# Performance work log

Hardware: AMD Instinct MI355X
Metric: run time of the kernel (lower is better)

Reference implementation:

```python
import jax, jax.numpy as jnp
import numpy as np

EPS = 1e-5  # torch BatchNorm2d default


def _conv5x5(x, w, b):
    # x: [N,1,H,W], w: [1,1,5,5], b: [1]; stride 1, padding 2 (SAME)
    out = jax.lax.conv_general_dilated(
        x, w, window_strides=(1, 1), padding=((2, 2), (2, 2)),
        dimension_numbers=("NCHW", "OIHW", "NCHW"))
    return out + b[None, :, None, None]


def _batchnorm(x, gamma, beta):
    # training-mode BatchNorm2d: per-channel batch stats over (N,H,W), biased var
    mean = jnp.mean(x, axis=(0, 2, 3), keepdims=True)
    var = jnp.mean(jnp.square(x - mean), axis=(0, 2, 3), keepdims=True)
    xhat = (x - mean) * jax.lax.rsqrt(var + EPS)
    return xhat * gamma[None, :, None, None] + beta[None, :, None, None]


def _shrinkage(x, lumdb):
    return x + 0.5 * (jnp.sqrt(jnp.square(x - lumdb) + 1.0)
                      - jnp.sqrt(jnp.square(x + lumdb) + 1.0))


def setup_inputs() -> dict:
    key = jax.random.key(0)
    k1, k2, k3 = jax.random.split(key, 3)
    y = jax.random.normal(k1, (64, 1, 512, 512), dtype=jnp.float32)
    # kaiming-uniform-ish init for a 1x1x5x5 conv
    fan_in = 25.0
    bound = 1.0 / np.sqrt(fan_in)
    conv_w = jax.random.uniform(k2, (1, 1, 5, 5), jnp.float32, -bound, bound)
    conv_b = jax.random.uniform(k3, (1,), jnp.float32, -bound, bound)
    gamma = jnp.ones((1,), jnp.float32)
    beta = jnp.zeros((1,), jnp.float32)
    lambd = jnp.array([2.0, 1.0, 0.0], jnp.float32)
    return {"y": y, "conv_w": conv_w, "conv_b": conv_b,
            "gamma": gamma, "beta": beta, "lambd": lambd}


def reference(y, conv_w, conv_b, gamma, beta, lambd):
    x_k = y
    # unrolled LISTA iteration 1
    x = _batchnorm(_conv5x5(x_k, conv_w, conv_b), gamma, beta)
    x = _shrinkage(x, lambd[0])
    o12 = _batchnorm(_conv5x5(x, conv_w, conv_b), gamma, beta)
    x = _batchnorm(_conv5x5(x_k, conv_w, conv_b), gamma, beta)
    # iteration 2
    x = _shrinkage(o12 + x, lambd[1])
    o22 = _batchnorm(_conv5x5(x, conv_w, conv_b), gamma, beta)
    x = _batchnorm(_conv5x5(x_k, conv_w, conv_b), gamma, beta)
    # iteration 3
    x = _shrinkage(o22 + x, lambd[2])
    return x
```

## Files before the change

kernel.cpp:

```cpp
#include <hip/hip_runtime.h>
#include <math.h>

#define HH 512
#define WW 512
#define NTOT (64u*512u*512u)
#define NBLK 1024
#define TS 128
#define TROWS 132
#define TCH 18
#define TPIT 152
#define NTASK (TROWS*TCH)
#define NITER 10

typedef __attribute__((ext_vector_type(8))) short short8;
typedef __attribute__((ext_vector_type(4))) float f32x4;

__device__ __forceinline__ float fsqrtf(float x) { return __builtin_amdgcn_sqrtf(x); }

__device__ __forceinline__ float shrinkf(float x, float l) {
    float a = x - l, b = x + l;
    return x + 0.5f * (fsqrtf(__builtin_fmaf(a, a, 1.f)) - fsqrtf(__builtin_fmaf(b, b, 1.f)));
}

__device__ __forceinline__ float bf2f(unsigned int u) {
    union { unsigned int i; float f; } cv;
    cv.i = u << 16;
    return cv.f;
}
__device__ __forceinline__ float lo2f(unsigned int p) {
    union { unsigned int i; float f; } cv; cv.i = p << 16; return cv.f;
}
__device__ __forceinline__ float hi2f(unsigned int p) {
    union { unsigned int i; float f; } cv; cv.i = p & 0xffff0000u; return cv.f;
}

__device__ __forceinline__ unsigned int cvtpk(float lo, float hi) {
    unsigned int r;
    asm("v_cvt_pk_bf16_f32 %0, %1, %2" : "=v"(r) : "v"(lo), "v"(hi));
    return r;
}

__device__ __forceinline__ void bf8(uint4 u, float* f) {
    f[0] = bf2f(u.x & 0xffffu); f[1] = bf2f(u.x >> 16);
    f[2] = bf2f(u.y & 0xffffu); f[3] = bf2f(u.y >> 16);
    f[4] = bf2f(u.z & 0xffffu); f[5] = bf2f(u.z >> 16);
    f[6] = bf2f(u.w & 0xffffu); f[7] = bf2f(u.w >> 16);
}

__device__ __forceinline__ void stats_reduce(
    const float* __restrict__ part, double* rs, double* rq, int tid,
    float gam, float bet, float& scl_out, float& shf_out)
{
    double sd = 0.0, qd = 0.0;
#pragma unroll
    for (int k = 0; k < 4; k++) {
        const int i = tid + k * 256;
        sd += (double)part[2 * i];
        qd += (double)part[2 * i + 1];
    }
    rs[tid] = sd; rq[tid] = qd;
    __syncthreads();
    for (int off = 128; off > 0; off >>= 1) {
        if (tid < off) { rs[tid] += rs[tid + off]; rq[tid] += rq[tid + off]; }
        __syncthreads();
    }
    const double mean = rs[0] / (double)NTOT;
    const double var  = rq[0] / (double)NTOT - mean * mean;
    const double scl  = (double)gam / sqrt(var + 1e-5);
    scl_out = (float)scl;
    shf_out = (float)((double)bet - mean * scl);
    __syncthreads();
}

template <int MODE, bool OBF>
__global__ __launch_bounds__(256, 4) void conv_k(
    const float* __restrict__ yin,
    const unsigned short* __restrict__ t1,
    const unsigned short* __restrict__ t2,
    unsigned short* __restrict__ outbf,
    float* __restrict__ outf32,
    const float* __restrict__ wgt,
    const float* __restrict__ bias,
    const float* __restrict__ prevPart,
    const float* __restrict__ statsIn,
    float* __restrict__ statsOut,
    const float* __restrict__ gamma,
    const float* __restrict__ beta,
    const float* __restrict__ lambd,
    float* __restrict__ partials)
{
    __shared__ unsigned short tile[TROWS * TPIT];

    const int tid = threadIdx.x;
    const int by = blockIdx.y * TS;
    const int bx = blockIdx.x * TS;
    const size_t ibase = (size_t)blockIdx.z * (HH * WW);

    float wloc[25];
#pragma unroll
    for (int i = 0; i < 25; i++) wloc[i] = wgt[i];

    const int lane = tid & 63;
    const int lm = lane & 15;
    const int kb = lane >> 4;
    const int basei = kb * 8 - lm - 6;
    short8 bfr[5];
#pragma unroll
    for (int ky = 0; ky < 5; ky++) {
        unsigned pkw[4];
#pragma unroll
        for (int jj = 0; jj < 4; jj++) {
            float v0 = 0.f, v1 = 0.f;
            const int i0 = basei + 2 * jj, i1 = i0 + 1;
#pragma unroll
            for (int t = 0; t < 5; t++) {
                if (i0 == t) v0 = wloc[ky * 5 + t];
                if (i1 == t) v1 = wloc[ky * 5 + t];
            }
            pkw[jj] = cvtpk(v0, v1);
        }
        union { unsigned u[4]; short8 s; } cv;
        cv.u[0] = pkw[0]; cv.u[1] = pkw[1]; cv.u[2] = pkw[2]; cv.u[3] = pkw[3];
        bfr[ky] = cv.s;
    }

    auto loadT = [&](int task, uint4& A, uint4& B) {
        A = make_uint4(0u,0u,0u,0u); B = make_uint4(0u,0u,0u,0u);
        const int row = task / TCH;
        const int ch  = task - row * TCH;
        const int gy  = by + row - 2;
        const int gx0 = bx + ch * 8 - 8;
        if (task < NTASK && gy >= 0 && gy < HH && gx0 >= 0 && gx0 <= WW - 8) {
            const size_t g = ibase + (size_t)gy * WW + gx0;
            if constexpr (MODE == 0) {
                A = *(const uint4*)(yin + g);
                B = *(const uint4*)(yin + g + 4);
            } else if constexpr (MODE == 1) {
                A = *(const uint4*)(t1 + g);
            } else {
                A = *(const uint4*)(t1 + g);
                B = *(const uint4*)(t2 + g);
            }
        }
    };

    uint4 sA0, sB0, sA1, sB1, sA2, sB2;
    loadT(tid,        sA0, sB0);
    loadT(tid + 256,  sA1, sB1);
    loadT(tid + 512,  sA2, sB2);

    float s1 = 0.f, h1 = 0.f, s2v = 0.f, h2 = 0.f, lam = 0.f;
    if constexpr (MODE == 1) {
        stats_reduce(prevPart, (double*)tile, ((double*)tile) + 256, tid,
                     gamma[0], beta[0], s1, h1);
        lam = lambd[0];
        if (tid == 0 && blockIdx.x == 0 && blockIdx.y == 0 && blockIdx.z == 0) {
            statsOut[0] = s1; statsOut[1] = h1;
        }
    }
    if constexpr (MODE == 2) {
        stats_reduce(prevPart, (double*)tile, ((double*)tile) + 256, tid,
                     gamma[0], beta[0], s2v, h2);
        s1 = statsIn[0]; h1 = statsIn[1];
        lam = lambd[1];
    }

    auto procT = [&](int task, uint4 A, uint4 B) {
        const int row = task / TCH;
        const int ch  = task - row * TCH;
        uint4 pk = make_uint4(0u,0u,0u,0u);
        if constexpr (MODE == 0) {
            const float4 a = *(const float4*)&A;
            const float4 b = *(const float4*)&B;
            pk.x = cvtpk(a.x, a.y); pk.y = cvtpk(a.z, a.w);
            pk.z = cvtpk(b.x, b.y); pk.w = cvtpk(b.z, b.w);
        } else if constexpr (MODE == 1) {
            float f1[8]; bf8(A, f1);
            float v[8];
#pragma unroll
            for (int k = 0; k < 8; k++)
                v[k] = shrinkf(__builtin_fmaf(f1[k], s1, h1), lam);
            pk.x = cvtpk(v[0], v[1]); pk.y = cvtpk(v[2], v[3]);
            pk.z = cvtpk(v[4], v[5]); pk.w = cvtpk(v[6], v[7]);
        } else {
            float f1[8], f2[8]; bf8(A, f1); bf8(B, f2);
            float v[8];
#pragma unroll
            for (int k = 0; k < 8; k++) {
                float x = __builtin_fmaf(f2[k], s2v, h2)
                        + __builtin_fmaf(f1[k], s1, h1);
                v[k] = shrinkf(x, lam);
            }
            pk.x = cvtpk(v[0], v[1]); pk.y = cvtpk(v[2], v[3]);
            pk.z = cvtpk(v[4], v[5]); pk.w = cvtpk(v[6], v[7]);
        }
        const int gy  = by + row - 2;
        const int gx0 = bx + ch * 8 - 8;
        if (!(gy >= 0 && gy < HH && gx0 >= 0 && gx0 <= WW - 8))
            pk = make_uint4(0u,0u,0u,0u);
        *(uint4*)&tile[row * TPIT + ch * 8] = pk;
    };

#pragma unroll
    for (int t = 0; t < NITER; t++) {
        const int task = tid + t * 256;
        if (task < NTASK) procT(task, sA0, sB0);
        sA0 = sA1; sB0 = sB1;
        sA1 = sA2; sB1 = sB2;
        if (t + 3 < NITER) {
            loadT(tid + (t + 3) * 256, sA2, sB2);
        } else {
            sA2 = make_uint4(0u,0u,0u,0u); sB2 = make_uint4(0u,0u,0u,0u);
        }
    }

    const float b0 = bias[0];
    __syncthreads();

    const int wv = tid >> 6;
    const int r0w = wv * 32;

    f32x4 acc[2][8];
#pragma unroll
    for (int st = 0; st < 2; st++)
#pragma unroll
        for (int ct = 0; ct < 8; ct++)
            acc[st][ct] = (f32x4){0.f, 0.f, 0.f, 0.f};

#pragma unroll
    for (int ky = 0; ky < 5; ky++) {
        const short8 b = bfr[ky];
#pragma unroll
        for (int st = 0; st < 2; st++) {
            const unsigned short* ab = &tile[(r0w + st * 16 + lm + ky) * TPIT + kb * 8];
#pragma unroll
            for (int ct = 0; ct < 8; ct++) {
                short8 a = *(const short8*)(ab + ct * 16);
                acc[st][ct] = __builtin_amdgcn_mfma_f32_16x16x32_bf16(a, b, acc[st][ct], 0, 0, 0);
            }
        }
    }

    float s = 0.f, q = 0.f;
#pragma unroll
    for (int st = 0; st < 2; st++) {
#pragma unroll
        for (int ct = 0; ct < 8; ct++) {
            const f32x4 a = acc[st][ct];
            const int grow0 = by + r0w + st * 16 + kb * 4;
            const size_t base = ibase + (size_t)grow0 * WW + bx + ct * 16 + lm;
            if constexpr (OBF) {
                unsigned p01 = cvtpk(a[0] + b0, a[1] + b0);
                unsigned p23 = cvtpk(a[2] + b0, a[3] + b0);
                outbf[base]          = (unsigned short)(p01 & 0xffffu);
                outbf[base + WW]     = (unsigned short)(p01 >> 16);
                outbf[base + 2 * WW] = (unsigned short)(p23 & 0xffffu);
                outbf[base + 3 * WW] = (unsigned short)(p23 >> 16);
                float fr0 = lo2f(p01), fr1 = hi2f(p01), fr2 = lo2f(p23), fr3 = hi2f(p23);
                s += fr0 + fr1 + fr2 + fr3;
                q = __builtin_fmaf(fr0, fr0, __builtin_fmaf(fr1, fr1,
                    __builtin_fmaf(fr2, fr2, __builtin_fmaf(fr3, fr3, q))));
            } else {
                float f0 = a[0] + b0, f1v = a[1] + b0, f2v = a[2] + b0, f3v = a[3] + b0;
                outf32[base]          = f0;
                outf32[base + WW]     = f1v;
                outf32[base + 2 * WW] = f2v;
                outf32[base + 3 * WW] = f3v;
                s += f0 + f1v + f2v + f3v;
                q = __builtin_fmaf(f0, f0, __builtin_fmaf(f1v, f1v,
                    __builtin_fmaf(f2v, f2v, __builtin_fmaf(f3v, f3v, q))));
            }
        }
    }

    __syncthreads();
    float* red = (float*)tile;
    red[tid] = s; red[256 + tid] = q;
    __syncthreads();
    for (int off = 128; off > 0; off >>= 1) {
        if (tid < off) { red[tid] += red[tid + off]; red[256 + tid] += red[256 + tid + off]; }
        __syncthreads();
    }
    if (tid == 0) {
        const int bid = (blockIdx.z * 4 + blockIdx.y) * 4 + blockIdx.x;
        partials[bid * 2] = red[0];
        partials[bid * 2 + 1] = red[256];
    }
}

template <bool T3BF>
__global__ __launch_bounds__(256) void final_k(
    const unsigned short* __restrict__ t1,
    const unsigned short* __restrict__ t3b,
    float* __restrict__ io,
    const float* __restrict__ p3,
    const float* __restrict__ statsIn,
    const float* __restrict__ gamma,
    const float* __restrict__ beta,
    const float* __restrict__ lambd)
{
    __shared__ double rbuf[512];
    const int tid = threadIdx.x;

    float s3, h3;
    stats_reduce(p3, rbuf, rbuf + 256, tid, gamma[0], beta[0], s3, h3);
    const float s1 = statsIn[0], h1 = statsIn[1];
    const float lam = lambd[2];

#pragma unroll
    for (int c = 0; c < 8; c++) {
        const size_t idx = ((size_t)c * 1024 + blockIdx.x) * 256 + tid;
        const size_t base = idx * 8;

        uint4 u1 = *(const uint4*)(t1 + base);
        float f1[8]; bf8(u1, f1);

        float t3v[8];
        if constexpr (T3BF) {
            uint4 u3 = *(const uint4*)(t3b + base);
            bf8(u3, t3v);
        } else {
            float4 a0 = *(const float4*)(io + base);
            float4 a1 = *(const float4*)(io + base + 4);
            t3v[0]=a0.x; t3v[1]=a0.y; t3v[2]=a0.z; t3v[3]=a0.w;
            t3v[4]=a1.x; t3v[5]=a1.y; t3v[6]=a1.z; t3v[7]=a1.w;
        }

        float r[8];
#pragma unroll
        for (int k = 0; k < 8; k++) {
            float v = __builtin_fmaf(t3v[k], s3, h3) + __builtin_fmaf(f1[k], s1, h1);
            r[k] = shrinkf(v, lam);
        }
        *(float4*)(io + base)     = make_float4(r[0], r[1], r[2], r[3]);
        *(float4*)(io + base + 4) = make_float4(r[4], r[5], r[6], r[7]);
    }
}

extern "C" void kernel_launch(void* const* d_in, const int* in_sizes, int n_in,
                              void* d_out, int out_size, void* d_ws, size_t ws_size,
                              hipStream_t stream)
{
    const float* y     = (const float*)d_in[0];
    const float* wgt   = (const float*)d_in[1];
    const float* bias  = (const float*)d_in[2];
    const float* gamma = (const float*)d_in[3];
    const float* beta  = (const float*)d_in[4];
    const float* lambd = (const float*)d_in[5];
    float* out = (float*)d_out;

    char* ws = (char*)d_ws;
    unsigned short* t1 = (unsigned short*)ws;
    unsigned short* t2 = (unsigned short*)(ws + 33554432ull);
    unsigned short* t3 = (unsigned short*)(ws + 67108864ull);
    const bool t3bf = (ws_size >= 100696088ull);
    const size_t poff = t3bf ? 100663296ull : 67108864ull;
    float* p1    = (float*)(ws + poff);
    float* p2    = (float*)(ws + poff + 8192ull);
    float* p3    = (float*)(ws + poff + 16384ull);
    float* stats = (float*)(ws + poff + 24576ull);

    dim3 grid(4, 4, 64), blk(256);
    conv_k<0, true><<<grid, blk, 0, stream>>>(y, nullptr, nullptr, t1, nullptr,
                                              wgt, bias, nullptr, nullptr, nullptr,
                                              gamma, beta, lambd, p1);
    conv_k<1, true><<<grid, blk, 0, stream>>>(nullptr, t1, nullptr, t2, nullptr,
                                              wgt, bias, p1, nullptr, stats,
                                              gamma, beta, lambd, p2);
    if (t3bf) {
        conv_k<2, true><<<grid, blk, 0, stream>>>(nullptr, t1, t2, t3, nullptr,
                                                  wgt, bias, p2, stats, nullptr,
                                                  gamma, beta, lambd, p3);
        final_k<true><<<1024, blk, 0, stream>>>(t1, t3, out, p3, stats,
                                                gamma, beta, lambd);
    } else {
        conv_k<2, false><<<grid, blk, 0, stream>>>(nullptr, t1, t2, nullptr, out,
                                                   wgt, bias, p2, stats, nullptr,
                                                   gamma, beta, lambd, p3);
        final_k<false><<<1024, blk, 0, stream>>>(t1, nullptr, out, p3, stats,
                                                 gamma, beta, lambd);
    }
}
```

Measured before the change: 97.84 us.

## Use wave-shuffle reductions for BN stats and swizzle block-to-tile mapping

Replaces the shared-memory tree reductions (many __syncthreads) for batch statistics with wave-level xor shuffles. Each wave now writes its own partial sums, which raises the partial count to 4096, and a single small shared buffer combines the four waves. The grid becomes 1D with a swizzled block index so that consecutive blocks land on different images and tiles, which may spread work differently across XCDs and caches. The trade-off is more global partials to read at the start of each kernel in exchange for fewer barriers.

```diff
diff --git a/kernel.cpp b/kernel.cpp
--- a/kernel.cpp
+++ b/kernel.cpp
@@ -4,13 +4,13 @@
 #define HH 512
 #define WW 512
 #define NTOT (64u*512u*512u)
-#define NBLK 1024
 #define TS 128
 #define TROWS 132
 #define TCH 18
 #define TPIT 152
 #define NTASK (TROWS*TCH)
 #define NITER 10
+#define NPART 4096
 
 typedef __attribute__((ext_vector_type(8))) short short8;
 typedef __attribute__((ext_vector_type(4))) float f32x4;
@@ -23,9 +23,7 @@
 }
 
 __device__ __forceinline__ float bf2f(unsigned int u) {
-    union { unsigned int i; float f; } cv;
-    cv.i = u << 16;
-    return cv.f;
+    union { unsigned int i; float f; } cv; cv.i = u << 16; return cv.f;
 }
 __device__ __forceinline__ float lo2f(unsigned int p) {
     union { unsigned int i; float f; } cv; cv.i = p << 16; return cv.f;
@@ -47,29 +45,32 @@
     f[6] = bf2f(u.w & 0xffffu); f[7] = bf2f(u.w >> 16);
 }
 
-__device__ __forceinline__ void stats_reduce(
-    const float* __restrict__ part, double* rs, double* rq, int tid,
+__device__ __forceinline__ void stats_fast(
+    const float* __restrict__ part, double* __restrict__ sbuf,
+    int tid, int lane, int wv,
     float gam, float bet, float& scl_out, float& shf_out)
 {
     double sd = 0.0, qd = 0.0;
 #pragma unroll
-    for (int k = 0; k < 4; k++) {
+    for (int k = 0; k < 16; k++) {
         const int i = tid + k * 256;
         sd += (double)part[2 * i];
         qd += (double)part[2 * i + 1];
     }
-    rs[tid] = sd; rq[tid] = qd;
+#pragma unroll
+    for (int off = 32; off > 0; off >>= 1) {
+        sd += __shfl_xor(sd, off);
+        qd += __shfl_xor(qd, off);
+    }
+    if (lane == 0) { sbuf[2 * wv] = sd; sbuf[2 * wv + 1] = qd; }
     __syncthreads();
-    for (int off = 128; off > 0; off >>= 1) {
-        if (tid < off) { rs[tid] += rs[tid + off]; rq[tid] += rq[tid + off]; }
-        __syncthreads();
-    }
-    const double mean = rs[0] / (double)NTOT;
-    const double var  = rq[0] / (double)NTOT - mean * mean;
+    const double S = sbuf[0] + sbuf[2] + sbuf[4] + sbuf[6];
+    const double Q = sbuf[1] + sbuf[3] + sbuf[5] + sbuf[7];
+    const double mean = S / (double)NTOT;
+    const double var  = Q / (double)NTOT - mean * mean;
     const double scl  = (double)gam / sqrt(var + 1e-5);
     scl_out = (float)scl;
     shf_out = (float)((double)bet - mean * scl);
-    __syncthreads();
 }
 
 template <int MODE, bool OBF>
@@ -90,19 +91,25 @@
     float* __restrict__ partials)
 {
     __shared__ unsigned short tile[TROWS * TPIT];
+    __shared__ double sbuf[8];
 
     const int tid = threadIdx.x;
-    const int by = blockIdx.y * TS;
-    const int bx = blockIdx.x * TS;
-    const size_t ibase = (size_t)blockIdx.z * (HH * WW);
-
-    float wloc[25];
-#pragma unroll
-    for (int i = 0; i < 25; i++) wloc[i] = wgt[i];
+    const int lin = blockIdx.x;
+    const int swz = ((lin & 7) << 7) | (lin >> 3);
+    const int img = swz >> 4;
+    const int rem = swz & 15;
+    const int by = ((rem >> 2) & 3) * TS;
+    const int bx = (rem & 3) * TS;
+    const size_t ibase = (size_t)img * (HH * WW);
 
     const int lane = tid & 63;
     const int lm = lane & 15;
     const int kb = lane >> 4;
+    const int wv = tid >> 6;
+
+    float wloc[25];
+#pragma unroll
+    for (int i = 0; i < 25; i++) wloc[i] = wgt[i];
     const int basei = kb * 8 - lm - 6;
     short8 bfr[5];
 #pragma unroll
@@ -120,7 +127,7 @@
             pkw[jj] = cvtpk(v0, v1);
         }
         union { unsigned u[4]; short8 s; } cv;
-        cv.u[0] = pkw[0]; cv.u[1] = pkw[1]; cv.u[2] = pkw[2]; cv.u[3] = pkw[3];
+        cv.u[0]=pkw[0]; cv.u[1]=pkw[1]; cv.u[2]=pkw[2]; cv.u[3]=pkw[3];
         bfr[ky] = cv.s;
     }
 
@@ -151,16 +158,12 @@
 
     float s1 = 0.f, h1 = 0.f, s2v = 0.f, h2 = 0.f, lam = 0.f;
     if constexpr (MODE == 1) {
-        stats_reduce(prevPart, (double*)tile, ((double*)tile) + 256, tid,
-                     gamma[0], beta[0], s1, h1);
+        stats_fast(prevPart, sbuf, tid, lane, wv, gamma[0], beta[0], s1, h1);
         lam = lambd[0];
-        if (tid == 0 && blockIdx.x == 0 && blockIdx.y == 0 && blockIdx.z == 0) {
-            statsOut[0] = s1; statsOut[1] = h1;
-        }
+        if (lin == 0 && tid == 0) { statsOut[0] = s1; statsOut[1] = h1; }
     }
     if constexpr (MODE == 2) {
-        stats_reduce(prevPart, (double*)tile, ((double*)tile) + 256, tid,
-                     gamma[0], beta[0], s2v, h2);
+        stats_fast(prevPart, sbuf, tid, lane, wv, gamma[0], beta[0], s2v, h2);
         s1 = statsIn[0]; h1 = statsIn[1];
         lam = lambd[1];
     }
@@ -207,17 +210,13 @@
         if (task < NTASK) procT(task, sA0, sB0);
         sA0 = sA1; sB0 = sB1;
         sA1 = sA2; sB1 = sB2;
-        if (t + 3 < NITER) {
-            loadT(tid + (t + 3) * 256, sA2, sB2);
-        } else {
-            sA2 = make_uint4(0u,0u,0u,0u); sB2 = make_uint4(0u,0u,0u,0u);
-        }
+        if (t + 3 < NITER) loadT(tid + (t + 3) * 256, sA2, sB2);
+        else { sA2 = make_uint4(0u,0u,0u,0u); sB2 = make_uint4(0u,0u,0u,0u); }
     }
 
     const float b0 = bias[0];
     __syncthreads();
 
-    const int wv = tid >> 6;
     const int r0w = wv * 32;
 
     f32x4 acc[2][8];
@@ -273,18 +272,14 @@
         }
     }
 
-    __syncthreads();
-    float* red = (float*)tile;
-    red[tid] = s; red[256 + tid] = q;
-    __syncthreads();
-    for (int off = 128; off > 0; off >>= 1) {
-        if (tid < off) { red[tid] += red[tid + off]; red[256 + tid] += red[256 + tid + off]; }
-        __syncthreads();
-    }
-    if (tid == 0) {
-        const int bid = (blockIdx.z * 4 + blockIdx.y) * 4 + blockIdx.x;
-        partials[bid * 2] = red[0];
-        partials[bid * 2 + 1] = red[256];
+#pragma unroll
+    for (int off = 32; off > 0; off >>= 1) {
+        s += __shfl_xor(s, off);
+        q += __shfl_xor(q, off);
+    }
+    if (lane == 0) {
+        partials[(swz * 4 + wv) * 2]     = s;
+        partials[(swz * 4 + wv) * 2 + 1] = q;
     }
 }
 
@@ -299,11 +294,13 @@
     const float* __restrict__ beta,
     const float* __restrict__ lambd)
 {
-    __shared__ double rbuf[512];
+    __shared__ double sbuf[8];
     const int tid = threadIdx.x;
+    const int lane = tid & 63;
+    const int wv = tid >> 6;
 
     float s3, h3;
-    stats_reduce(p3, rbuf, rbuf + 256, tid, gamma[0], beta[0], s3, h3);
+    stats_fast(p3, sbuf, tid, lane, wv, gamma[0], beta[0], s3, h3);
     const float s1 = statsIn[0], h1 = statsIn[1];
     const float lam = lambd[2];
 
@@ -353,14 +350,14 @@
     unsigned short* t1 = (unsigned short*)ws;
     unsigned short* t2 = (unsigned short*)(ws + 33554432ull);
     unsigned short* t3 = (unsigned short*)(ws + 67108864ull);
-    const bool t3bf = (ws_size >= 100696088ull);
+    const bool t3bf = (ws_size >= 100761608ull);
     const size_t poff = t3bf ? 100663296ull : 67108864ull;
     float* p1    = (float*)(ws + poff);
-    float* p2    = (float*)(ws + poff + 8192ull);
-    float* p3    = (float*)(ws + poff + 16384ull);
-    float* stats = (float*)(ws + poff + 24576ull);
-
-    dim3 grid(4, 4, 64), blk(256);
+    float* p2    = (float*)(ws + poff + 32768ull);
+    float* p3    = (float*)(ws + poff + 65536ull);
+    float* stats = (float*)(ws + poff + 98304ull);
+
+    dim3 grid(1024, 1, 1), blk(256, 1, 1);
     conv_k<0, true><<<grid, blk, 0, stream>>>(y, nullptr, nullptr, t1, nullptr,
                                               wgt, bias, nullptr, nullptr, nullptr,
                                               gamma, beta, lambd, p1);
@@ -371,13 +368,13 @@
         conv_k<2, true><<<grid, blk, 0, stream>>>(nullptr, t1, t2, t3, nullptr,
                                                   wgt, bias, p2, stats, nullptr,
                                                   gamma, beta, lambd, p3);
-        final_k<true><<<1024, blk, 0, stream>>>(t1, t3, out, p3, stats,
+        final_k<true><<<grid, blk, 0, stream>>>(t1, t3, out, p3, stats,
                                                 gamma, beta, lambd);
     } else {
         conv_k<2, false><<<grid, blk, 0, stream>>>(nullptr, t1, t2, nullptr, out,
                                                    wgt, bias, p2, stats, nullptr,
                                                    gamma, beta, lambd, p3);
-        final_k<false><<<1024, blk, 0, stream>>>(t1, nullptr, out, p3, stats,
+        final_k<false><<<grid, blk, 0, stream>>>(t1, nullptr, out, p3, stats,
                                                  gamma, beta, lambd);
     }
 }
```

New measurement: 91.30 us (median of 2 runs). 6.7% less time.
